# Kernel tuning notes

Measured on AMD Instinct MI355X. Metric: run time of the kernel, lower is better.

Reference implementation:

```python
import jax, jax.numpy as jnp
import numpy as np

N = 100000   # nodes
E = 1600000  # edges
D = 64       # in = hidden channels
L = 4        # num_layers
G = 512      # graphs in batch
OUT = 10     # out_channels
EPS = 1e-5   # batch-norm eps


def setup_inputs() -> dict:
    key = jax.random.key(0)
    ks = jax.random.split(key, 10)
    x = jax.random.normal(ks[0], (N, D), jnp.float32)
    edge_index = jax.random.randint(ks[1], (2, E), 0, N, dtype=jnp.int32)
    batch = jnp.sort(jax.random.randint(ks[2], (N,), 0, G, dtype=jnp.int32))
    Ws = jax.random.normal(ks[3], (L, D, D), jnp.float32) * 0.1   # GCNConv weights
    bs = jax.random.normal(ks[4], (L, D), jnp.float32) * 0.01     # GCNConv biases
    W1 = jax.random.normal(ks[5], (L * D, D), jnp.float32) * 0.1  # MLP hidden lin
    b1 = jnp.zeros((D,), jnp.float32)
    gamma = jnp.ones((D,), jnp.float32)   # MLP BatchNorm affine
    beta = jnp.zeros((D,), jnp.float32)
    W2 = jax.random.normal(ks[6], (D, OUT), jnp.float32) * 0.1    # MLP out lin
    b2 = jnp.zeros((OUT,), jnp.float32)
    return {"x": x, "edge_index": edge_index, "batch": batch, "Ws": Ws, "bs": bs,
            "W1": W1, "b1": b1, "gamma": gamma, "beta": beta, "W2": W2, "b2": b2}


def reference(x, edge_index, batch, Ws, bs, W1, b1, gamma, beta, W2, b2):
    src, dst = edge_index[0], edge_index[1]
    # symmetric GCN normalization with self-loops (improved=False -> weight 1)
    deg = jax.ops.segment_sum(jnp.ones((E,), x.dtype), dst, num_segments=N) + 1.0
    dis = jax.lax.rsqrt(deg)                 # deg^{-1/2}, finite since deg >= 1
    enorm = dis[src] * dis[dst]              # per-edge coefficient
    snorm = dis * dis                        # self-loop coefficient

    h = x
    pooled = []
    for l in range(L):  # no activation between convs, as in the source
        hw = h @ Ws[l]                                                   # [N, D]
        agg = jax.ops.segment_sum(hw[src] * enorm[:, None], dst, num_segments=N)
        h = agg + hw * snorm[:, None] + bs[l]
        pooled.append(jax.ops.segment_sum(h, batch, num_segments=G))     # [G, D]
    z = jnp.concatenate(pooled, axis=1)                                  # [G, L*D]

    # PyG MLP([L*D, D, OUT], act='relu'): lin -> batch_norm -> relu -> lin
    z = z @ W1 + b1
    mean = z.mean(axis=0)
    var = z.var(axis=0)
    z = (z - mean) * jax.lax.rsqrt(var + EPS) * gamma + beta
    z = jax.nn.relu(z)
    return z @ W2 + b2
```

## Files before the change

kernel.cpp:

```cpp
#include <hip/hip_runtime.h>

#define NN   100000
#define NE   1600000
#define DD   64
#define LL   4
#define GG   512
#define OUTC 10
#define EPSV 1e-5f
#define PARTSZ 12500

#define OFF_RS    0
#define OFF_CSR   100016
#define OFF_BUFA  1700016
#define OFF_BUFB  8100016
#define OFF_POOL  14500016

static __device__ __forceinline__ unsigned short f2bf(float f) {
    unsigned int u = __float_as_uint(f);
    unsigned int r = (u + 0x7fffu + ((u >> 16) & 1u)) >> 16;
    return (unsigned short)r;
}
static __device__ __forceinline__ float plo(unsigned int v) {
    return __uint_as_float(v << 16);
}
static __device__ __forceinline__ float phi(unsigned int v) {
    return __uint_as_float(v & 0xffff0000u);
}

__global__ void deg_part_kernel(const int* __restrict__ dst, int* __restrict__ deg) {
    int p   = blockIdx.x & 7;
    int sub = blockIdx.x >> 3;
    int nb  = gridDim.x >> 3;
    for (int e = sub * 256 + threadIdx.x; e < NE; e += nb * 256) {
        int d = dst[e];
        if (d / PARTSZ == p) atomicAdd(&deg[d], 1);
    }
}

__global__ void scan1_kernel(const int* __restrict__ deg, int* __restrict__ loc,
                             int* __restrict__ bsum) {
    int t = threadIdx.x;
    int i = blockIdx.x * 1024 + t;
    int v = (i < NN) ? deg[i] : 0;
    __shared__ int ps[1024];
    ps[t] = v;
    __syncthreads();
    #pragma unroll
    for (int off = 1; off < 1024; off <<= 1) {
        int u = (t >= off) ? ps[t - off] : 0;
        __syncthreads();
        ps[t] += u;
        __syncthreads();
    }
    if (i < NN) loc[i] = ps[t] - v;
    if (t == 1023) bsum[blockIdx.x] = ps[1023];
}

__global__ void scan2_kernel(const int* __restrict__ bsum, int* __restrict__ boff) {
    int t = threadIdx.x;
    int v = (t < 98) ? bsum[t] : 0;
    __shared__ int ps[128];
    ps[t] = v;
    __syncthreads();
    #pragma unroll
    for (int off = 1; off < 128; off <<= 1) {
        int u = (t >= off) ? ps[t - off] : 0;
        __syncthreads();
        ps[t] += u;
        __syncthreads();
    }
    if (t < 98) boff[t] = ps[t] - v;
    if (t == 127) boff[98] = ps[127];
}

__global__ void scan3_kernel(const int* __restrict__ loc, const int* __restrict__ boff,
                             int* __restrict__ rs) {
    int i = blockIdx.x * 1024 + threadIdx.x;
    if (i < NN) rs[i] = loc[i] + boff[i >> 10];
    if (i == NN) rs[NN] = boff[98];
}

__global__ void fill_part_kernel(const int* __restrict__ src, const int* __restrict__ dst,
                                 const int* __restrict__ rs, int* __restrict__ cnt,
                                 int* __restrict__ csr) {
    int p   = blockIdx.x & 7;
    int sub = blockIdx.x >> 3;
    int nb  = gridDim.x >> 3;
    for (int e = sub * 256 + threadIdx.x; e < NE; e += nb * 256) {
        int d = dst[e];
        if (d / PARTSZ == p) {
            int slot = rs[d] + atomicAdd(&cnt[d], 1);
            csr[slot] = src[e];
        }
    }
}

__global__ void t0_kernel(const float* __restrict__ x, const int* __restrict__ rs,
                          unsigned short* __restrict__ t0) {
    int i = blockIdx.x * 256 + threadIdx.x;
    int n = i >> 4;
    float di = rsqrtf((float)(rs[n + 1] - rs[n]) + 1.0f);
    float4 v = ((const float4*)x)[i];
    ushort4 o;
    o.x = f2bf(v.x * di); o.y = f2bf(v.y * di);
    o.z = f2bf(v.z * di); o.w = f2bf(v.w * di);
    ((ushort4*)t0)[i] = o;
}

__global__ __launch_bounds__(256)
void gather_kernel(const unsigned short* __restrict__ t, const int* __restrict__ csr,
                   const int* __restrict__ rs, unsigned short* __restrict__ vout) {
    const uint2* tu2 = (const uint2*)t;
    uint2* vo2 = (uint2*)vout;
    int tid = threadIdx.x;
    int nwg = gridDim.x;
    int q = nwg >> 3, r = nwg & 7;
    int xcd = blockIdx.x & 7, sub = blockIdx.x >> 3;
    int bid = (xcd < r ? xcd * (q + 1) : r * (q + 1) + (xcd - r) * q) + sub;

    int n = bid * 16 + (tid >> 4);
    int l = tid & 15;
    int j0 = rs[n], j1 = rs[n + 1];
    float di = rsqrtf((float)(j1 - j0) + 1.0f);

    uint2 sv = tu2[n * 16 + l];
    float a0 = plo(sv.x), a1 = phi(sv.x), a2 = plo(sv.y), a3 = phi(sv.y);

    int j = j0;
    #pragma clang loop unroll(disable)
    for (; j + 7 < j1; j += 8) {
        int i0 = csr[j],     i1 = csr[j + 1], i2 = csr[j + 2], i3 = csr[j + 3];
        int i4 = csr[j + 4], i5 = csr[j + 5], i6 = csr[j + 6], i7 = csr[j + 7];
        uint2 v0 = tu2[i0 * 16 + l];
        uint2 v1 = tu2[i1 * 16 + l];
        uint2 v2 = tu2[i2 * 16 + l];
        uint2 v3 = tu2[i3 * 16 + l];
        uint2 v4 = tu2[i4 * 16 + l];
        uint2 v5 = tu2[i5 * 16 + l];
        uint2 v6 = tu2[i6 * 16 + l];
        uint2 v7 = tu2[i7 * 16 + l];
        a0 += ((plo(v0.x) + plo(v1.x)) + (plo(v2.x) + plo(v3.x)))
            + ((plo(v4.x) + plo(v5.x)) + (plo(v6.x) + plo(v7.x)));
        a1 += ((phi(v0.x) + phi(v1.x)) + (phi(v2.x) + phi(v3.x)))
            + ((phi(v4.x) + phi(v5.x)) + (phi(v6.x) + phi(v7.x)));
        a2 += ((plo(v0.y) + plo(v1.y)) + (plo(v2.y) + plo(v3.y)))
            + ((plo(v4.y) + plo(v5.y)) + (plo(v6.y) + plo(v7.y)));
        a3 += ((phi(v0.y) + phi(v1.y)) + (phi(v2.y) + phi(v3.y)))
            + ((phi(v4.y) + phi(v5.y)) + (phi(v6.y) + phi(v7.y)));
    }
    #pragma clang loop unroll(disable)
    for (; j + 3 < j1; j += 4) {
        int i0 = csr[j], i1 = csr[j + 1], i2 = csr[j + 2], i3 = csr[j + 3];
        uint2 v0 = tu2[i0 * 16 + l];
        uint2 v1 = tu2[i1 * 16 + l];
        uint2 v2 = tu2[i2 * 16 + l];
        uint2 v3 = tu2[i3 * 16 + l];
        a0 += (plo(v0.x) + plo(v1.x)) + (plo(v2.x) + plo(v3.x));
        a1 += (phi(v0.x) + phi(v1.x)) + (phi(v2.x) + phi(v3.x));
        a2 += (plo(v0.y) + plo(v1.y)) + (plo(v2.y) + plo(v3.y));
        a3 += (phi(v0.y) + phi(v1.y)) + (phi(v2.y) + phi(v3.y));
    }
    #pragma clang loop unroll(disable)
    for (; j < j1; ++j) {
        uint2 v0 = tu2[csr[j] * 16 + l];
        a0 += plo(v0.x); a1 += phi(v0.x);
        a2 += plo(v0.y); a3 += phi(v0.y);
    }
    uint2 o;
    o.x = (unsigned int)f2bf(a0 * di) | ((unsigned int)f2bf(a1 * di) << 16);
    o.y = (unsigned int)f2bf(a2 * di) | ((unsigned int)f2bf(a3 * di) << 16);
    vo2[n * 16 + l] = o;
}

__global__ __launch_bounds__(256)
void vgemm_kernel(const unsigned short* __restrict__ v, const float* __restrict__ W,
                  const float* __restrict__ bias, const int* __restrict__ rs,
                  const int* __restrict__ batch, unsigned short* __restrict__ tout,
                  float* __restrict__ pooled, int l, int last) {
    __shared__ float Wsh[64 * 64];
    __shared__ float hs[16][64];
    __shared__ float red[4][64];
    const uint2* vu2 = (const uint2*)v;
    int tid = threadIdx.x;
    #pragma unroll
    for (int i = 0; i < 16; ++i) Wsh[tid + i * 256] = W[tid + i * 256];
    int w = tid >> 6, d = tid & 63;
    float bd = bias[d];

    for (int c = blockIdx.x; c < NN / 16; c += gridDim.x) {
        int n0 = c * 16;
        {
            int rr = tid >> 4, cc = tid & 15;
            uint2 u = vu2[(n0 + rr) * 16 + cc];
            hs[rr][4 * cc]     = plo(u.x);
            hs[rr][4 * cc + 1] = phi(u.x);
            hs[rr][4 * cc + 2] = plo(u.y);
            hs[rr][4 * cc + 3] = phi(u.y);
        }
        __syncthreads();
        float a0 = 0.f, a1 = 0.f, a2 = 0.f, a3 = 0.f;
        #pragma unroll 2
        for (int k4 = 0; k4 < 16; ++k4) {
            float4 h0 = *(const float4*)&hs[w * 4 + 0][k4 * 4];
            float4 h1 = *(const float4*)&hs[w * 4 + 1][k4 * 4];
            float4 h2 = *(const float4*)&hs[w * 4 + 2][k4 * 4];
            float4 h3 = *(const float4*)&hs[w * 4 + 3][k4 * 4];
            float w0 = Wsh[(k4 * 4 + 0) * 64 + d];
            float w1 = Wsh[(k4 * 4 + 1) * 64 + d];
            float w2 = Wsh[(k4 * 4 + 2) * 64 + d];
            float w3 = Wsh[(k4 * 4 + 3) * 64 + d];
            a0 = fmaf(h0.x, w0, a0); a0 = fmaf(h0.y, w1, a0);
            a0 = fmaf(h0.z, w2, a0); a0 = fmaf(h0.w, w3, a0);
            a1 = fmaf(h1.x, w0, a1); a1 = fmaf(h1.y, w1, a1);
            a1 = fmaf(h1.z, w2, a1); a1 = fmaf(h1.w, w3, a1);
            a2 = fmaf(h2.x, w0, a2); a2 = fmaf(h2.y, w1, a2);
            a2 = fmaf(h2.z, w2, a2); a2 = fmaf(h2.w, w3, a2);
            a3 = fmaf(h3.x, w0, a3); a3 = fmaf(h3.y, w1, a3);
            a3 = fmaf(h3.z, w2, a3); a3 = fmaf(h3.w, w3, a3);
        }
        float accs[4] = {a0, a1, a2, a3};
        if (!last) {
            #pragma unroll
            for (int s = 0; s < 4; ++s) {
                int n = n0 + w * 4 + s;
                float di = rsqrtf((float)(rs[n + 1] - rs[n]) + 1.0f);
                tout[n * 64 + d] = f2bf((accs[s] + bd) * di);
            }
        }
        int glo = batch[n0], ghi = batch[n0 + 15];
        if (glo == ghi) {
            red[w][d] = ((a0 + a1) + (a2 + a3)) + 4.0f * bd;
            __syncthreads();
            if (w == 0) {
                float tot = (red[0][d] + red[1][d]) + (red[2][d] + red[3][d]);
                atomicAdd(&pooled[glo * 256 + l * 64 + d], tot);
            }
        } else {
            #pragma unroll
            for (int s = 0; s < 4; ++s) {
                int n = n0 + w * 4 + s;
                atomicAdd(&pooled[batch[n] * 256 + l * 64 + d], accs[s] + bd);
            }
        }
        __syncthreads();
    }
}

__global__ void mlp1_kernel(const float* __restrict__ pooled, const float* __restrict__ W1,
                            const float* __restrict__ b1, float* __restrict__ z1,
                            float* __restrict__ sums) {
    __shared__ float row[256];
    int g = blockIdx.x, d = threadIdx.x;
    #pragma unroll
    for (int i = 0; i < 4; ++i) row[d + i * 64] = pooled[g * 256 + d + i * 64];
    __syncthreads();
    float acc = b1[d];
    #pragma unroll 8
    for (int k = 0; k < 256; ++k) acc = fmaf(row[k], W1[k * 64 + d], acc);
    z1[g * 64 + d] = acc;
    atomicAdd(&sums[d], acc);
    atomicAdd(&sums[64 + d], acc * acc);
}

__global__ void mlp2_kernel(const float* __restrict__ z1, const float* __restrict__ sums,
                            const float* __restrict__ gamma, const float* __restrict__ beta,
                            const float* __restrict__ W2, const float* __restrict__ b2,
                            float* __restrict__ out) {
    int g = blockIdx.x, d = threadIdx.x;
    float mean = sums[d] * (1.0f / 512.0f);
    float var  = sums[64 + d] * (1.0f / 512.0f) - mean * mean;
    float z = (z1[g * 64 + d] - mean) * rsqrtf(var + EPSV) * gamma[d] + beta[d];
    z = fmaxf(z, 0.0f);
    #pragma unroll
    for (int o = 0; o < OUTC; ++o) {
        float v = z * W2[d * OUTC + o];
        #pragma unroll
        for (int s = 32; s; s >>= 1) v += __shfl_xor(v, s, 64);
        if (d == 0) out[g * OUTC + o] = v + b2[o];
    }
}

extern "C" void kernel_launch(void* const* d_in, const int* in_sizes, int n_in,
                              void* d_out, int out_size, void* d_ws, size_t ws_size,
                              hipStream_t stream) {
    (void)in_sizes; (void)n_in; (void)out_size; (void)ws_size;
    const float* x     = (const float*)d_in[0];
    const int*   ei    = (const int*)d_in[1];
    const int*   src   = ei;
    const int*   dst   = ei + NE;
    const int*   batch = (const int*)d_in[2];
    const float* Wc    = (const float*)d_in[3];
    const float* bc    = (const float*)d_in[4];
    const float* W1    = (const float*)d_in[5];
    const float* b1    = (const float*)d_in[6];
    const float* gamma = (const float*)d_in[7];
    const float* beta  = (const float*)d_in[8];
    const float* W2    = (const float*)d_in[9];
    const float* b2    = (const float*)d_in[10];
    float* out = (float*)d_out;
    float* ws  = (float*)d_ws;

    int*   rs     = (int*)(ws + OFF_RS);
    int*   csr    = (int*)(ws + OFF_CSR);
    int*   loc    = (int*)(ws + OFF_CSR);
    unsigned short* tping = (unsigned short*)(ws + OFF_BUFA);
    unsigned short* vbuf  = tping + 6400000;
    unsigned short* tpong = (unsigned short*)(ws + OFF_BUFB);
    float* pooled = ws + OFF_POOL;
    int*   degcnt = (int*)(ws + OFF_POOL);
    int*   bsum   = (int*)(ws + OFF_BUFA);
    int*   boff   = (int*)(ws + OFF_BUFA) + 128;
    float* z1     = ws + OFF_BUFA;
    float* sums   = ws + OFF_BUFA + GG * DD;

    hipMemsetAsync(degcnt, 0, NN * sizeof(int), stream);
    deg_part_kernel<<<1024, 256, 0, stream>>>(dst, degcnt);
    scan1_kernel<<<98, 1024, 0, stream>>>(degcnt, loc, bsum);
    scan2_kernel<<<1, 128, 0, stream>>>(bsum, boff);
    scan3_kernel<<<99, 1024, 0, stream>>>(loc, boff, rs);
    hipMemsetAsync(degcnt, 0, NN * sizeof(int), stream);
    fill_part_kernel<<<1024, 256, 0, stream>>>(src, dst, rs, degcnt, csr);

    t0_kernel<<<NN * 16 / 256, 256, 0, stream>>>(x, rs, tping);
    hipMemsetAsync(pooled, 0, GG * LL * DD * sizeof(float), stream);

    unsigned short* tin = tping; unsigned short* tot = tpong;
    for (int l = 0; l < LL; ++l) {
        gather_kernel<<<NN / 16, 256, 0, stream>>>(tin, csr, rs, vbuf);
        vgemm_kernel<<<1536, 256, 0, stream>>>(vbuf, Wc + l * 4096, bc + l * 64,
                                               rs, batch, tot, pooled,
                                               l, l == LL - 1);
        unsigned short* tmp = tin; tin = tot; tot = tmp;
    }

    hipMemsetAsync(sums, 0, 128 * sizeof(float), stream);
    mlp1_kernel<<<GG, 64, 0, stream>>>(pooled, W1, b1, z1, sums);
    mlp2_kernel<<<GG, 64, 0, stream>>>(z1, sums, gamma, beta, W2, b2, out);
}
```

Baseline: 493.0 us.

## Bucket edges by destination partition before degree count and CSR fill

Adds a pre-pass that packs each edge into a 32-bit key (local dst, src) and scatters it into one of eight per-partition staging buffers. The degree and fill kernels then read only their own bucket instead of each of eight block groups scanning all edges and filtering by partition. This cuts the eightfold redundant reads of dst/src, at the cost of an extra scatter pass and staging buffer that reuses the pong buffer. The vgemm grid is also halved from 1536 to 768 blocks.

```diff
diff --git a/kernel.cpp b/kernel.cpp
--- a/kernel.cpp
+++ b/kernel.cpp
@@ -8,6 +8,7 @@
 #define OUTC 10
 #define EPSV 1e-5f
 #define PARTSZ 12500
+#define CAP   250000
 
 #define OFF_RS    0
 #define OFF_CSR   100016
@@ -27,13 +28,53 @@
     return __uint_as_float(v & 0xffff0000u);
 }
 
-__global__ void deg_part_kernel(const int* __restrict__ dst, int* __restrict__ deg) {
-    int p   = blockIdx.x & 7;
+__global__ __launch_bounds__(256)
+void bucket_kernel(const int* __restrict__ src, const int* __restrict__ dst,
+                   int* __restrict__ bucketCnt, unsigned int* __restrict__ staging) {
+    __shared__ int hist[8];
+    __shared__ int base[8];
+    int tid = threadIdx.x;
+    if (tid < 8) hist[tid] = 0;
+    __syncthreads();
+    int e0 = blockIdx.x * 1024 + tid * 4;
+    int b0 = 0, b1 = 0, b2 = 0, b3 = 0, p0 = 0, p1 = 0, p2 = 0, p3 = 0;
+    unsigned int k0 = 0, k1 = 0, k2 = 0, k3 = 0;
+    bool ok = (e0 < NE);
+    if (ok) {
+        int4 d4 = *(const int4*)&dst[e0];
+        int4 s4 = *(const int4*)&src[e0];
+        b0 = d4.x / PARTSZ; k0 = ((unsigned int)(d4.x - b0 * PARTSZ) << 17) | (unsigned int)s4.x;
+        b1 = d4.y / PARTSZ; k1 = ((unsigned int)(d4.y - b1 * PARTSZ) << 17) | (unsigned int)s4.y;
+        b2 = d4.z / PARTSZ; k2 = ((unsigned int)(d4.z - b2 * PARTSZ) << 17) | (unsigned int)s4.z;
+        b3 = d4.w / PARTSZ; k3 = ((unsigned int)(d4.w - b3 * PARTSZ) << 17) | (unsigned int)s4.w;
+        p0 = atomicAdd(&hist[b0], 1);
+        p1 = atomicAdd(&hist[b1], 1);
+        p2 = atomicAdd(&hist[b2], 1);
+        p3 = atomicAdd(&hist[b3], 1);
+    }
+    __syncthreads();
+    if (tid < 8) base[tid] = atomicAdd(&bucketCnt[tid], hist[tid]);
+    __syncthreads();
+    if (ok) {
+        staging[b0 * CAP + base[b0] + p0] = k0;
+        staging[b1 * CAP + base[b1] + p1] = k1;
+        staging[b2 * CAP + base[b2] + p2] = k2;
+        staging[b3 * CAP + base[b3] + p3] = k3;
+    }
+}
+
+__global__ __launch_bounds__(256)
+void deg_bucket_kernel(const unsigned int* __restrict__ staging,
+                       const int* __restrict__ bucketCnt, int* __restrict__ deg) {
+    int b   = blockIdx.x & 7;
     int sub = blockIdx.x >> 3;
     int nb  = gridDim.x >> 3;
-    for (int e = sub * 256 + threadIdx.x; e < NE; e += nb * 256) {
-        int d = dst[e];
-        if (d / PARTSZ == p) atomicAdd(&deg[d], 1);
+    int cnt = bucketCnt[b];
+    const unsigned int* st = staging + b * CAP;
+    int dbase = b * PARTSZ;
+    for (int i = sub * 256 + threadIdx.x; i < cnt; i += nb * 256) {
+        unsigned int v = st[i];
+        atomicAdd(&deg[dbase + (v >> 17)], 1);
     }
 }
 
@@ -80,18 +121,21 @@
     if (i == NN) rs[NN] = boff[98];
 }
 
-__global__ void fill_part_kernel(const int* __restrict__ src, const int* __restrict__ dst,
-                                 const int* __restrict__ rs, int* __restrict__ cnt,
-                                 int* __restrict__ csr) {
-    int p   = blockIdx.x & 7;
+__global__ __launch_bounds__(256)
+void fill_bucket_kernel(const unsigned int* __restrict__ staging,
+                        const int* __restrict__ bucketCnt, const int* __restrict__ rs,
+                        int* __restrict__ cnt, int* __restrict__ csr) {
+    int b   = blockIdx.x & 7;
     int sub = blockIdx.x >> 3;
     int nb  = gridDim.x >> 3;
-    for (int e = sub * 256 + threadIdx.x; e < NE; e += nb * 256) {
-        int d = dst[e];
-        if (d / PARTSZ == p) {
-            int slot = rs[d] + atomicAdd(&cnt[d], 1);
-            csr[slot] = src[e];
-        }
+    int n   = bucketCnt[b];
+    const unsigned int* st = staging + b * CAP;
+    int dbase = b * PARTSZ;
+    for (int i = sub * 256 + threadIdx.x; i < n; i += nb * 256) {
+        unsigned int v = st[i];
+        int d = dbase + (int)(v >> 17);
+        int slot = rs[d] + atomicAdd(&cnt[d], 1);
+        csr[slot] = (int)(v & 0x1FFFFu);
     }
 }
 
@@ -300,12 +344,14 @@
     float* out = (float*)d_out;
     float* ws  = (float*)d_ws;
 
-    int*   rs     = (int*)(ws + OFF_RS);
-    int*   csr    = (int*)(ws + OFF_CSR);
-    int*   loc    = (int*)(ws + OFF_CSR);
+    int*   rs        = (int*)(ws + OFF_RS);
+    int*   bucketCnt = (int*)(ws + OFF_RS) + 100004;
+    int*   csr       = (int*)(ws + OFF_CSR);
+    int*   loc       = (int*)(ws + OFF_CSR);
     unsigned short* tping = (unsigned short*)(ws + OFF_BUFA);
     unsigned short* vbuf  = tping + 6400000;
     unsigned short* tpong = (unsigned short*)(ws + OFF_BUFB);
+    unsigned int* staging = (unsigned int*)(ws + OFF_BUFB);
     float* pooled = ws + OFF_POOL;
     int*   degcnt = (int*)(ws + OFF_POOL);
     int*   bsum   = (int*)(ws + OFF_BUFA);
@@ -313,13 +359,15 @@
     float* z1     = ws + OFF_BUFA;
     float* sums   = ws + OFF_BUFA + GG * DD;
 
+    hipMemsetAsync(bucketCnt, 0, 8 * sizeof(int), stream);
     hipMemsetAsync(degcnt, 0, NN * sizeof(int), stream);
-    deg_part_kernel<<<1024, 256, 0, stream>>>(dst, degcnt);
+    bucket_kernel<<<(NE + 1023) / 1024, 256, 0, stream>>>(src, dst, bucketCnt, staging);
+    deg_bucket_kernel<<<1024, 256, 0, stream>>>(staging, bucketCnt, degcnt);
     scan1_kernel<<<98, 1024, 0, stream>>>(degcnt, loc, bsum);
     scan2_kernel<<<1, 128, 0, stream>>>(bsum, boff);
     scan3_kernel<<<99, 1024, 0, stream>>>(loc, boff, rs);
     hipMemsetAsync(degcnt, 0, NN * sizeof(int), stream);
-    fill_part_kernel<<<1024, 256, 0, stream>>>(src, dst, rs, degcnt, csr);
+    fill_bucket_kernel<<<1024, 256, 0, stream>>>(staging, bucketCnt, rs, degcnt, csr);
 
     t0_kernel<<<NN * 16 / 256, 256, 0, stream>>>(x, rs, tping);
     hipMemsetAsync(pooled, 0, GG * LL * DD * sizeof(float), stream);
@@ -327,9 +375,9 @@
     unsigned short* tin = tping; unsigned short* tot = tpong;
     for (int l = 0; l < LL; ++l) {
         gather_kernel<<<NN / 16, 256, 0, stream>>>(tin, csr, rs, vbuf);
-        vgemm_kernel<<<1536, 256, 0, stream>>>(vbuf, Wc + l * 4096, bc + l * 64,
-                                               rs, batch, tot, pooled,
-                                               l, l == LL - 1);
+        vgemm_kernel<<<768, 256, 0, stream>>>(vbuf, Wc + l * 4096, bc + l * 64,
+                                              rs, batch, tot, pooled,
+                                              l, l == LL - 1);
         unsigned short* tmp = tin; tin = tot; tot = tmp;
     }
 
```

After: 519.5 us. 1.05x slower.
